# Kernel tuning notes

Measured on AMD Instinct MI355X. Metric: run time of the kernel, lower is better.

Reference implementation:

```python
import jax, jax.numpy as jnp
import numpy as np

A, B, I, H, O = 400, 64, 50, 192, 3   # num_agents, batch, input_dim, hidden_dim, output_dim
ADIM, NH = 128, 8                      # attention_dim, num_heads
HD = ADIM // NH
SCALE = HD ** -0.5
EPS = 1e-5


def _ln(x, g, b):
    mu = jnp.mean(x, -1, keepdims=True)
    v = jnp.mean((x - mu) ** 2, -1, keepdims=True)
    return (x - mu) * jax.lax.rsqrt(v + EPS) * g + b


def setup_inputs() -> dict:
    key = jax.random.key(0)
    ks = jax.random.split(key, 12)
    s = 0.05
    n = lambda k, shape: (jax.random.normal(k, shape, jnp.float32) * s)
    return {
        'x': jax.random.normal(ks[0], (B, I), jnp.float32),
        'ln_in_g': jnp.ones((A, I), jnp.float32), 'ln_in_b': jnp.zeros((A, I), jnp.float32),
        'W1': n(ks[1], (A, I, H)), 'b1': jnp.zeros((A, H), jnp.float32),
        'Ws1': n(ks[2], (A, I, H)), 'bs1': jnp.zeros((A, H), jnp.float32),
        'W2': n(ks[3], (A, H, H)), 'b2': jnp.zeros((A, H), jnp.float32),
        'Ws2': n(ks[4], (A, H, H)), 'bs2': jnp.zeros((A, H), jnp.float32),
        'W3': n(ks[5], (A, H, H)), 'b3': jnp.zeros((A, H), jnp.float32),
        'ln_h_g': jnp.ones((A, H), jnp.float32), 'ln_h_b': jnp.zeros((A, H), jnp.float32),
        'Wout': n(ks[6], (A, H, O)), 'bout': jnp.zeros((A, O), jnp.float32),
        'aln_g': jnp.ones((H,), jnp.float32), 'aln_b': jnp.zeros((H,), jnp.float32),
        'Wq': n(ks[7], (H, ADIM)), 'bq': jnp.zeros((ADIM,), jnp.float32),
        'Wk': n(ks[8], (H, ADIM)), 'bk': jnp.zeros((ADIM,), jnp.float32),
        'Wv': n(ks[9], (H, ADIM)), 'bv': jnp.zeros((ADIM,), jnp.float32),
        'Wo': n(ks[10], (ADIM, H)), 'bo': jnp.zeros((H,), jnp.float32),
    }


def _forward(x, ln_in_g, ln_in_b, W1, b1, Ws1, bs1, W2, b2, Ws2, bs2, W3, b3,
             ln_h_g, ln_h_b, Wout, bout, aln_g, aln_b, Wq, bq, Wk, bk, Wv, bv, Wo, bo):
    gelu = lambda t: jax.nn.gelu(t, approximate=False)  # torch F.gelu default = exact erf
    # per-agent input LayerNorm (shared stats, per-agent affine) -> [A, B, I]
    xn = _ln(x[None, :, :], ln_in_g[:, None, :], ln_in_b[:, None, :])
    # agent MLPs as batched GEMMs over agent axis
    h1 = gelu(jnp.einsum('abi,aih->abh', xn, W1) + b1[:, None, :]) \
         + jnp.einsum('abi,aih->abh', xn, Ws1) + bs1[:, None, :]
    h2 = gelu(jnp.einsum('abh,ahk->abk', h1, W2) + b2[:, None, :]) \
         + jnp.einsum('abh,ahk->abk', h1, Ws2) + bs2[:, None, :]
    h3 = _ln(h2 + jnp.einsum('abh,ahk->abk', h2, W3) + b3[:, None, :],
             ln_h_g[:, None, :], ln_h_b[:, None, :])  # [A, B, H]
    # cross-SREK attention across the agent axis
    y = _ln(h3, aln_g, aln_b)
    q = (y @ Wq + bq).reshape(A, B, NH, HD).transpose(1, 2, 0, 3)  # [B, NH, A, HD]
    k = (y @ Wk + bk).reshape(A, B, NH, HD).transpose(1, 2, 0, 3)
    v = (y @ Wv + bv).reshape(A, B, NH, HD).transpose(1, 2, 0, 3)
    attn = jax.nn.softmax(jnp.einsum('bhad,bhcd->bhac', q, k) * SCALE, axis=-1)
    o = jnp.einsum('bhac,bhcd->bhad', attn, v).transpose(2, 0, 1, 3).reshape(A, B, ADIM)
    attended = h3 + (o @ Wo + bo)  # residual (dropout off in eval)
    # per-agent output heads -> [A, B, O]
    logits = jnp.einsum('abh,aho->abo', attended, Wout) + bout[:, None, :]
    return logits


def reference(x, ln_in_g, ln_in_b, W1, b1, Ws1, bs1, W2, b2, Ws2, bs2, W3, b3,
              ln_h_g, ln_h_b, Wout, bout, aln_g, aln_b, Wq, bq, Wk, bk, Wv, bv, Wo, bo):
    return _forward(x, ln_in_g, ln_in_b, W1, b1, Ws1, bs1, W2, b2, Ws2, bs2, W3, b3,
                    ln_h_g, ln_h_b, Wout, bout, aln_g, aln_b, Wq, bq, Wk, bk, Wv, bv, Wo, bo)
```

## Files before the change

### kernel.cpp

```cpp
#include <hip/hip_runtime.h>
#include <math.h>

#define AGENTS 400
#define BATCH  64
#define IDIM   50
#define HDIM   192
#define ODIM   3
#define ADIMM  128
#define NHEADS 8
#define HEADD  16
#define LN_EPS 1e-5f

#define PA   200
#define PAM  192
#define POUT 136

typedef __bf16 bf16x8 __attribute__((ext_vector_type(8)));
typedef float  f32x4  __attribute__((ext_vector_type(4)));

__device__ __forceinline__ float gelu_exact(float x) {
    return 0.5f * x * (1.0f + erff(x * 0.70710678118654752f));
}

__device__ __forceinline__ unsigned pack_bf16x2(float a, float b) {
    unsigned short ua = __builtin_bit_cast(unsigned short, (__bf16)a);
    unsigned short ub = __builtin_bit_cast(unsigned short, (__bf16)b);
    return (unsigned)ua | ((unsigned)ub << 16);
}

__device__ __forceinline__ int as_swz(int row, int col) {
    return ((((col >> 3) ^ (row & 7)) << 3) | (col & 7));
}
__device__ __forceinline__ void st_as(__bf16* As_, int row, int col, float v) {
    As_[row * PAM + as_swz(row, col)] = (__bf16)v;
}
__device__ __forceinline__ float ld_as(const __bf16* As_, int row, int col) {
    return (float)As_[row * PAM + as_swz(row, col)];
}
__device__ __forceinline__ bf16x8 ld_afrag(const __bf16* As_, int row, int k0) {
    int blk = (((k0 >> 3) ^ (row & 7)) << 3);
    return *(const bf16x8*)&As_[row * PAM + blk];
}

template<int NC, int KD>
__device__ __forceinline__ void mlp_gemm2(f32x4 (&acc1)[4][3], f32x4 (&acc2)[4][3],
                                          const float* __restrict__ W,
                                          const float* __restrict__ Ws,
                                          const __bf16* As_, int n0, int lane)
{
    const int r = lane & 15, g = lane >> 4;
    const int colb[3] = { n0 + r, n0 + 16 + r, n0 + 32 + r };
    float b1f[24], b2f[24];

    #pragma unroll
    for (int t = 0; t < 3; t++)
        #pragma unroll
        for (int j = 0; j < 8; j++) {
            int k = g * 8 + j;
            int off = k * HDIM + colb[t];
            b1f[t * 8 + j] = (k < KD) ? W[off]  : 0.f;
            b2f[t * 8 + j] = (k < KD) ? Ws[off] : 0.f;
        }

    #pragma unroll
    for (int c = 0; c < NC; c++) {
        bf16x8 bf1[3], bf2[3];
        #pragma unroll
        for (int t = 0; t < 3; t++)
            #pragma unroll
            for (int j = 0; j < 8; j++) {
                bf1[t][j] = (__bf16)b1f[t * 8 + j];
                bf2[t][j] = (__bf16)b2f[t * 8 + j];
            }
        if (c + 1 < NC) {
            #pragma unroll
            for (int t = 0; t < 3; t++)
                #pragma unroll
                for (int j = 0; j < 8; j++) {
                    int k = (c + 1) * 32 + g * 8 + j;
                    int off = k * HDIM + colb[t];
                    b1f[t * 8 + j] = (k < KD) ? W[off]  : 0.f;
                    b2f[t * 8 + j] = (k < KD) ? Ws[off] : 0.f;
                }
        }
        #pragma unroll
        for (int rg = 0; rg < 4; rg++) {
            bf16x8 af = ld_afrag(As_, 16 * rg + r, c * 32 + g * 8);
            #pragma unroll
            for (int t = 0; t < 3; t++) {
                acc1[rg][t] = __builtin_amdgcn_mfma_f32_16x16x32_bf16(af, bf1[t], acc1[rg][t], 0, 0, 0);
                acc2[rg][t] = __builtin_amdgcn_mfma_f32_16x16x32_bf16(af, bf2[t], acc2[rg][t], 0, 0, 0);
            }
        }
    }
}

template<int NC, int KD>
__device__ __forceinline__ void mlp_gemm1(f32x4 (&acc)[4][3],
                                          const float* __restrict__ W,
                                          const __bf16* As_, int n0, int lane)
{
    const int r = lane & 15, g = lane >> 4;
    const int colb[3] = { n0 + r, n0 + 16 + r, n0 + 32 + r };
    float bf[24];

    #pragma unroll
    for (int t = 0; t < 3; t++)
        #pragma unroll
        for (int j = 0; j < 8; j++) {
            int k = g * 8 + j;
            bf[t * 8 + j] = (k < KD) ? W[k * HDIM + colb[t]] : 0.f;
        }

    #pragma unroll
    for (int c = 0; c < NC; c++) {
        bf16x8 bfr[3];
        #pragma unroll
        for (int t = 0; t < 3; t++)
            #pragma unroll
            for (int j = 0; j < 8; j++)
                bfr[t][j] = (__bf16)bf[t * 8 + j];
        if (c + 1 < NC) {
            #pragma unroll
            for (int t = 0; t < 3; t++)
                #pragma unroll
                for (int j = 0; j < 8; j++) {
                    int k = (c + 1) * 32 + g * 8 + j;
                    bf[t * 8 + j] = (k < KD) ? W[k * HDIM + colb[t]] : 0.f;
                }
        }
        #pragma unroll
        for (int rg = 0; rg < 4; rg++) {
            bf16x8 af = ld_afrag(As_, 16 * rg + r, c * 32 + g * 8);
            #pragma unroll
            for (int t = 0; t < 3; t++)
                acc[rg][t] = __builtin_amdgcn_mfma_f32_16x16x32_bf16(af, bfr[t], acc[rg][t], 0, 0, 0);
        }
    }
}

__global__ __launch_bounds__(256, 2) void mlp_kernel(
    const float* __restrict__ x,
    const float* __restrict__ ln_in_g, const float* __restrict__ ln_in_b,
    const float* __restrict__ W1, const float* __restrict__ b1,
    const float* __restrict__ Ws1, const float* __restrict__ bs1,
    const float* __restrict__ W2, const float* __restrict__ b2,
    const float* __restrict__ Ws2, const float* __restrict__ bs2,
    const float* __restrict__ W3, const float* __restrict__ b3,
    const float* __restrict__ ln_h_g, const float* __restrict__ ln_h_b,
    float* __restrict__ h3out)
{
    const int a    = blockIdx.x;
    const int tid  = threadIdx.x;
    const int wave = tid >> 6, lane = tid & 63;
    const int r = lane & 15, g = lane >> 4;
    const int n0 = 48 * wave;

    __shared__ __align__(16) __bf16 As[64 * PAM];
    __shared__ float mu_s[64], rs_s[64];

    {
        int rr = tid >> 2, l = tid & 3;
        float s = 0.f, ss = 0.f;
        for (int k = l; k < IDIM; k += 4) { float v = x[rr * IDIM + k]; s += v; ss += v * v; }
        s  += __shfl_down(s, 2, 4);  s  += __shfl_down(s, 1, 4);
        ss += __shfl_down(ss, 2, 4); ss += __shfl_down(ss, 1, 4);
        if (l == 0) {
            float mu = s * (1.0f / IDIM);
            float var = ss * (1.0f / IDIM) - mu * mu;
            mu_s[rr] = mu;
            rs_s[rr] = rsqrtf(var + LN_EPS);
        }
    }
    __syncthreads();
    for (int sidx = tid; sidx < 64 * 64; sidx += 256) {
        int rr = sidx >> 6, k = sidx & 63;
        float v = 0.f;
        if (k < IDIM)
            v = (x[rr * IDIM + k] - mu_s[rr]) * rs_s[rr] * ln_in_g[a * IDIM + k] + ln_in_b[a * IDIM + k];
        st_as(As, rr, k, v);
    }
    __syncthreads();

    const float* W1p  = W1  + (size_t)a * IDIM * HDIM;
    const float* Ws1p = Ws1 + (size_t)a * IDIM * HDIM;
    const float* W2p  = W2  + (size_t)a * HDIM * HDIM;
    const float* Ws2p = Ws2 + (size_t)a * HDIM * HDIM;
    const float* W3p  = W3  + (size_t)a * HDIM * HDIM;

    {
        f32x4 acc1[4][3], acc2[4][3];
        #pragma unroll
        for (int i = 0; i < 4; i++)
            #pragma unroll
            for (int t = 0; t < 3; t++) { acc1[i][t] = (f32x4)0.f; acc2[i][t] = (f32x4)0.f; }
        mlp_gemm2<2, IDIM>(acc1, acc2, W1p, Ws1p, As, n0, lane);
        __syncthreads();
        #pragma unroll
        for (int t = 0; t < 3; t++) {
            int col = n0 + 16 * t + r;
            float bb  = b1[a * HDIM + col];
            float bbs = bs1[a * HDIM + col];
            #pragma unroll
            for (int rg = 0; rg < 4; rg++)
                #pragma unroll
                for (int i = 0; i < 4; i++) {
                    int row = 16 * rg + 4 * g + i;
                    st_as(As, row, col, gelu_exact(acc1[rg][t][i] + bb) + acc2[rg][t][i] + bbs);
                }
        }
        __syncthreads();
    }

    {
        f32x4 acc1[4][3], acc2[4][3];
        #pragma unroll
        for (int i = 0; i < 4; i++)
            #pragma unroll
            for (int t = 0; t < 3; t++) { acc1[i][t] = (f32x4)0.f; acc2[i][t] = (f32x4)0.f; }
        mlp_gemm2<6, HDIM>(acc1, acc2, W2p, Ws2p, As, n0, lane);
        __syncthreads();
        #pragma unroll
        for (int t = 0; t < 3; t++) {
            int col = n0 + 16 * t + r;
            float bb  = b2[a * HDIM + col];
            float bbs = bs2[a * HDIM + col];
            #pragma unroll
            for (int rg = 0; rg < 4; rg++)
                #pragma unroll
                for (int i = 0; i < 4; i++) {
                    int row = 16 * rg + 4 * g + i;
                    st_as(As, row, col, gelu_exact(acc1[rg][t][i] + bb) + acc2[rg][t][i] + bbs);
                }
        }
        __syncthreads();
    }

    {
        f32x4 acc[4][3];
        #pragma unroll
        for (int i = 0; i < 4; i++)
            #pragma unroll
            for (int t = 0; t < 3; t++) acc[i][t] = (f32x4)0.f;
        mlp_gemm1<6, HDIM>(acc, W3p, As, n0, lane);
        __syncthreads();
        #pragma unroll
        for (int t = 0; t < 3; t++) {
            int col = n0 + 16 * t + r;
            float bb = b3[a * HDIM + col];
            #pragma unroll
            for (int rg = 0; rg < 4; rg++)
                #pragma unroll
                for (int i = 0; i < 4; i++) {
                    int row = 16 * rg + 4 * g + i;
                    st_as(As, row, col, ld_as(As, row, col) + acc[rg][t][i] + bb);
                }
        }
        __syncthreads();
    }

    {
        int rr = tid >> 2, l = tid & 3;
        float s = 0.f, ss = 0.f;
        for (int k = l; k < HDIM; k += 4) { float v = ld_as(As, rr, k); s += v; ss += v * v; }
        s  += __shfl_down(s, 2, 4);  s  += __shfl_down(s, 1, 4);
        ss += __shfl_down(ss, 2, 4); ss += __shfl_down(ss, 1, 4);
        if (l == 0) {
            float mu = s * (1.0f / HDIM);
            float var = ss * (1.0f / HDIM) - mu * mu;
            mu_s[rr] = mu;
            rs_s[rr] = rsqrtf(var + LN_EPS);
        }
    }
    __syncthreads();
    for (int sidx = tid; sidx < 64 * 48; sidx += 256) {
        int rr = sidx / 48, q = sidx - rr * 48;
        int c = q * 4;
        const __bf16* p = &As[rr * PAM + as_swz(rr, c)];
        float4 gv = *(const float4*)&ln_h_g[a * HDIM + c];
        float4 bv = *(const float4*)&ln_h_b[a * HDIM + c];
        float mu = mu_s[rr], rs = rs_s[rr];
        float4 o;
        o.x = ((float)p[0] - mu) * rs * gv.x + bv.x;
        o.y = ((float)p[1] - mu) * rs * gv.y + bv.y;
        o.z = ((float)p[2] - mu) * rs * gv.z + bv.z;
        o.w = ((float)p[3] - mu) * rs * gv.w + bv.w;
        *(float4*)&h3out[((size_t)a * BATCH + rr) * HDIM + c] = o;
    }
}

template<int NC, int KD, int NT, int NRG, int LDW, int PITCH>
__device__ __forceinline__ void gemm_bpass(f32x4 (&acc)[NRG][NT],
                                           const float* const* wptr,
                                           const __bf16* Asrc, int lane)
{
    const int r = lane & 15, g = lane >> 4;
    float buf[2][NT * 8];

    #pragma unroll
    for (int t = 0; t < NT; t++)
        #pragma unroll
        for (int j = 0; j < 8; j++) {
            int k = g * 8 + j;
            buf[0][t * 8 + j] = (k < KD) ? wptr[t][k * LDW + r] : 0.f;
        }

    #pragma unroll
    for (int c = 0; c < NC; c++) {
        const int cur = c & 1, nxt = cur ^ 1;
        if (c + 1 < NC) {
            #pragma unroll
            for (int t = 0; t < NT; t++)
                #pragma unroll
                for (int j = 0; j < 8; j++) {
                    int k = (c + 1) * 32 + g * 8 + j;
                    buf[nxt][t * 8 + j] = (k < KD) ? wptr[t][k * LDW + r] : 0.f;
                }
        }
        bf16x8 bfr[NT];
        #pragma unroll
        for (int t = 0; t < NT; t++)
            #pragma unroll
            for (int j = 0; j < 8; j++)
                bfr[t][j] = (__bf16)buf[cur][t * 8 + j];
        #pragma unroll
        for (int rg = 0; rg < NRG; rg++) {
            bf16x8 af = *(const bf16x8*)&Asrc[(16 * rg + r) * PITCH + c * 32 + g * 8];
            #pragma unroll
            for (int t = 0; t < NT; t++)
                acc[rg][t] = __builtin_amdgcn_mfma_f32_16x16x32_bf16(af, bfr[t], acc[rg][t], 0, 0, 0);
        }
    }
}

__global__ __launch_bounds__(256, 2) void qkv_kernel(
    const float* __restrict__ h3,
    const float* __restrict__ aln_g, const float* __restrict__ aln_b,
    const float* __restrict__ Wq, const float* __restrict__ bq,
    const float* __restrict__ Wk, const float* __restrict__ bk,
    const float* __restrict__ Wv, const float* __restrict__ bv,
    float* __restrict__ qT, float* __restrict__ kT, float* __restrict__ vT)
{
    const int a    = blockIdx.x;
    const int tid  = threadIdx.x;
    const int wave = tid >> 6, lane = tid & 63;
    const int r = lane & 15, g = lane >> 4;

    __shared__ __align__(16) __bf16 ys[64 * PA];
    __shared__ float mu_s[64], rs_s[64];

    {
        int rr = tid >> 2, l = tid & 3;
        const float* hp = h3 + ((size_t)a * BATCH + rr) * HDIM;
        float s = 0.f, ss = 0.f;
        for (int k = l; k < HDIM; k += 4) { float v = hp[k]; s += v; ss += v * v; }
        s  += __shfl_down(s, 2, 4);  s  += __shfl_down(s, 1, 4);
        ss += __shfl_down(ss, 2, 4); ss += __shfl_down(ss, 1, 4);
        if (l == 0) {
            float mu = s * (1.0f / HDIM);
            float var = ss * (1.0f / HDIM) - mu * mu;
            mu_s[rr] = mu;
            rs_s[rr] = rsqrtf(var + LN_EPS);
        }
    }
    __syncthreads();
    for (int sidx = tid; sidx < 64 * HDIM; sidx += 256) {
        int rr = sidx / HDIM, c = sidx - rr * HDIM;
        float v = (h3[((size_t)a * BATCH + rr) * HDIM + c] - mu_s[rr]) * rs_s[rr] * aln_g[c] + aln_b[c];
        ys[rr * PA + c] = (__bf16)v;
    }
    __syncthreads();

    #pragma unroll
    for (int p = 0; p < 2; p++) {
        const int nb = 192 * p + 48 * wave;
        const float* wA[3];
        #pragma unroll
        for (int t = 0; t < 3; t++) {
            int nt = nb + 16 * t;
            const float* base = (nt < 128) ? Wq : (nt < 256) ? Wk : Wv;
            wA[t] = base + (nt & 127);
        }
        f32x4 acc[4][3];
        #pragma unroll
        for (int i = 0; i < 4; i++)
            #pragma unroll
            for (int t = 0; t < 3; t++) acc[i][t] = (f32x4)0.f;
        gemm_bpass<6, HDIM, 3, 4, ADIMM, PA>(acc, wA, ys, lane);

        #pragma unroll
        for (int t = 0; t < 3; t++) {
            int n = nb + 16 * t + r;
            int which = n >> 7, cc = n & 127, hh = cc >> 4, dd = cc & 15;
            const float* bp = (which == 0) ? bq : (which == 1) ? bk : bv;
            float* op = (which == 0) ? qT : (which == 1) ? kT : vT;
            float bb = bp[cc];
            #pragma unroll
            for (int rg = 0; rg < 4; rg++)
                #pragma unroll
                for (int i = 0; i < 4; i++) {
                    int brow = 16 * rg + 4 * g + i;
                    op[(((size_t)brow * NHEADS + hh) * AGENTS + a) * HEADD + dd] = acc[rg][t][i] + bb;
                }
        }
    }
}

#define PKA 24
#define PVA 408
#define PPA 232

__global__ __launch_bounds__(256, 2) void attn_kernel(
    const float* __restrict__ qT, const float* __restrict__ kT,
    const float* __restrict__ vT, float* __restrict__ oT)
{
    const int bh   = blockIdx.x;
    const int b    = bh >> 3, h = bh & 7;
    const int tid  = threadIdx.x;
    const int wave = tid >> 6, lane = tid & 63;
    const int r = lane & 15, g = lane >> 4;

    __shared__ __align__(16) __bf16 Ks[AGENTS * PKA];
    __shared__ __align__(16) __bf16 Vt[16 * PVA];
    __shared__ __align__(16) __bf16 Ps[4][16 * PPA];

    const float* kp = kT + (size_t)bh * AGENTS * HEADD;
    const float* vp = vT + (size_t)bh * AGENTS * HEADD;
    for (int idx = tid; idx < AGENTS * HEADD; idx += 256) {
        int a_ = idx >> 4, d = idx & 15;
        Ks[a_ * PKA + d] = (__bf16)kp[idx];
        Vt[d * PVA + a_] = (__bf16)vp[idx];
    }
    __bf16* Pw = Ps[wave];
    for (int z = lane; z < 16 * 16; z += 64)
        Pw[(z >> 4) * PPA + 208 + (z & 15)] = (__bf16)0.f;
    __syncthreads();

    for (int mt = wave; mt < 25; mt += 4) {
        const int m0 = mt * 16;

        bf16x8 aq;
        if (g < 2) {
            const float* qp = qT + ((size_t)bh * AGENTS + m0 + r) * HEADD + g * 8;
            #pragma unroll
            for (int j = 0; j < 8; j++) aq[j] = (__bf16)(qp[j] * 0.25f);
        } else {
            #pragma unroll
            for (int j = 0; j < 8; j++) aq[j] = (__bf16)0.f;
        }

        f32x4 sacc[25];
        #pragma unroll
        for (int t = 0; t < 25; t++) {
            bf16x8 bk_ = *(const bf16x8*)&Ks[(t * 16 + r) * PKA + (g & 1) * 8];
            sacc[t] = __builtin_amdgcn_mfma_f32_16x16x32_bf16(aq, bk_, (f32x4)0.f, 0, 0, 0);
        }

        float lv[4];
        #pragma unroll
        for (int i = 0; i < 4; i++) {
            float m_ = sacc[0][i];
            #pragma unroll
            for (int t = 1; t < 25; t++) m_ = fmaxf(m_, sacc[t][i]);
            #pragma unroll
            for (int off = 8; off; off >>= 1) m_ = fmaxf(m_, __shfl_xor(m_, off, 16));
            float l_ = 0.f;
            #pragma unroll
            for (int t = 0; t < 25; t++) {
                float p = __expf(sacc[t][i] - m_);
                sacc[t][i] = p;
                l_ += p;
            }
            #pragma unroll
            for (int off = 8; off; off >>= 1) l_ += __shfl_xor(l_, off, 16);
            lv[i] = l_;
        }

        f32x4 oacc = (f32x4)0.f;

        #pragma unroll
        for (int t = 0; t < 13; t++)
            #pragma unroll
            for (int i = 0; i < 4; i++)
                Pw[(g * 4 + i) * PPA + t * 16 + r] = (__bf16)sacc[t][i];
        __asm__ volatile("s_waitcnt lgkmcnt(0)" ::: "memory");
        #pragma unroll
        for (int c = 0; c < 7; c++) {
            bf16x8 ap  = *(const bf16x8*)&Pw[r * PPA + c * 32 + g * 8];
            bf16x8 bv_ = *(const bf16x8*)&Vt[r * PVA + c * 32 + g * 8];
            oacc = __builtin_amdgcn_mfma_f32_16x16x32_bf16(ap, bv_, oacc, 0, 0, 0);
        }

        for (int z = lane; z < 16 * 16; z += 64)
            Pw[(z >> 4) * PPA + 192 + (z & 15)] = (__bf16)0.f;
        #pragma unroll
        for (int t = 13; t < 25; t++)
            #pragma unroll
            for (int i = 0; i < 4; i++)
                Pw[(g * 4 + i) * PPA + (t - 13) * 16 + r] = (__bf16)sacc[t][i];
        __asm__ volatile("s_waitcnt lgkmcnt(0)" ::: "memory");
        #pragma unroll
        for (int c = 0; c < 6; c++) {
            bf16x8 ap  = *(const bf16x8*)&Pw[r * PPA + c * 32 + g * 8];
            bf16x8 bv_ = *(const bf16x8*)&Vt[r * PVA + 208 + c * 32 + g * 8];
            oacc = __builtin_amdgcn_mfma_f32_16x16x32_bf16(ap, bv_, oacc, 0, 0, 0);
        }

        #pragma unroll
        for (int i = 0; i < 4; i++)
            oT[((size_t)(m0 + g * 4 + i) * BATCH + b) * ADIMM + h * HEADD + r] = oacc[i] / lv[i];
    }
}

__global__ __launch_bounds__(256, 2) void out_kernel(
    const float* __restrict__ h3, const float* __restrict__ oT,
    const float* __restrict__ Wo, const float* __restrict__ bo,
    const float* __restrict__ Wout, const float* __restrict__ bout,
    float* __restrict__ out)
{
    const int a    = blockIdx.x;
    const int tid  = threadIdx.x;
    const int wave = tid >> 6, lane = tid & 63;
    const int r = lane & 15, g = lane >> 4;
    const int n0 = 48 * wave;

    __shared__ __align__(16) __bf16 os[64 * POUT];
    __shared__ __align__(16) __bf16 att[64 * PA];

    for (int idx = tid; idx < 64 * 32; idx += 256) {
        int bb = idx >> 5, q = idx & 31;
        float4 v = ((const float4*)(oT + ((size_t)a * BATCH + bb) * ADIMM))[q];
        unsigned u0 = pack_bf16x2(v.x, v.y);
        unsigned u1 = pack_bf16x2(v.z, v.w);
        *(uint2*)&os[bb * POUT + q * 4] = make_uint2(u0, u1);
    }
    __syncthreads();

    {
        const float* wA[3] = { Wo + n0, Wo + n0 + 16, Wo + n0 + 32 };
        f32x4 acc[4][3];
        #pragma unroll
        for (int i = 0; i < 4; i++)
            #pragma unroll
            for (int t = 0; t < 3; t++) acc[i][t] = (f32x4)0.f;
        gemm_bpass<4, ADIMM, 3, 4, HDIM, POUT>(acc, wA, os, lane);
        #pragma unroll
        for (int t = 0; t < 3; t++) {
            int col = n0 + 16 * t + r;
            float bb = bo[col];
            #pragma unroll
            for (int rg = 0; rg < 4; rg++)
                #pragma unroll
                for (int i = 0; i < 4; i++) {
                    int row = 16 * rg + 4 * g + i;
                    float v = h3[((size_t)a * BATCH + row) * HDIM + col] + acc[rg][t][i] + bb;
                    att[row * PA + col] = (__bf16)v;
                }
        }
    }
    __syncthreads();

    {
        const float* Wp = Wout + (size_t)a * HDIM * ODIM;
        float wb[48];
        #pragma unroll
        for (int c = 0; c < 6; c++)
            #pragma unroll
            for (int j = 0; j < 8; j++) {
                int k = c * 32 + g * 8 + j;
                wb[c * 8 + j] = (r < ODIM) ? Wp[k * ODIM + r] : 0.f;
            }
        f32x4 oacc = (f32x4)0.f;
        #pragma unroll
        for (int c = 0; c < 6; c++) {
            bf16x8 bf;
            #pragma unroll
            for (int j = 0; j < 8; j++) bf[j] = (__bf16)wb[c * 8 + j];
            bf16x8 af = *(const bf16x8*)&att[(16 * wave + r) * PA + c * 32 + g * 8];
            oacc = __builtin_amdgcn_mfma_f32_16x16x32_bf16(af, bf, oacc, 0, 0, 0);
        }
        if (r < ODIM) {
            float bb = bout[a * ODIM + r];
            #pragma unroll
            for (int i = 0; i < 4; i++) {
                int row = 16 * wave + 4 * g + i;
                out[((size_t)a * BATCH + row) * ODIM + r] = oacc[i] + bb;
            }
        }
    }
}

extern "C" void kernel_launch(void* const* d_in, const int* in_sizes, int n_in,
                              void* d_out, int out_size, void* d_ws, size_t ws_size,
                              hipStream_t stream)
{
    const float* x       = (const float*)d_in[0];
    const float* ln_in_g = (const float*)d_in[1];
    const float* ln_in_b = (const float*)d_in[2];
    const float* W1      = (const float*)d_in[3];
    const float* b1      = (const float*)d_in[4];
    const float* Ws1     = (const float*)d_in[5];
    const float* bs1     = (const float*)d_in[6];
    const float* W2      = (const float*)d_in[7];
    const float* b2      = (const float*)d_in[8];
    const float* Ws2     = (const float*)d_in[9];
    const float* bs2     = (const float*)d_in[10];
    const float* W3      = (const float*)d_in[11];
    const float* b3      = (const float*)d_in[12];
    const float* ln_h_g  = (const float*)d_in[13];
    const float* ln_h_b  = (const float*)d_in[14];
    const float* Wout    = (const float*)d_in[15];
    const float* bout    = (const float*)d_in[16];
    const float* aln_g   = (const float*)d_in[17];
    const float* aln_b   = (const float*)d_in[18];
    const float* Wq      = (const float*)d_in[19];
    const float* bq      = (const float*)d_in[20];
    const float* Wk      = (const float*)d_in[21];
    const float* bk      = (const float*)d_in[22];
    const float* Wv      = (const float*)d_in[23];
    const float* bv      = (const float*)d_in[24];
    const float* Wo      = (const float*)d_in[25];
    const float* bo      = (const float*)d_in[26];
    float* out = (float*)d_out;

    float* ws = (float*)d_ws;
    const size_t H3_SZ = (size_t)AGENTS * BATCH * HDIM;
    const size_t QT_SZ = (size_t)BATCH * NHEADS * AGENTS * HEADD;
    float* h3 = ws;
    float* qT = h3 + H3_SZ;
    float* kT = qT + QT_SZ;
    float* vT = kT + QT_SZ;
    float* oT = vT + QT_SZ;

    mlp_kernel<<<AGENTS, 256, 0, stream>>>(x, ln_in_g, ln_in_b,
                                           W1, b1, Ws1, bs1, W2, b2, Ws2, bs2,
                                           W3, b3, ln_h_g, ln_h_b, h3);
    qkv_kernel<<<AGENTS, 256, 0, stream>>>(h3, aln_g, aln_b,
                                           Wq, bq, Wk, bk, Wv, bv, qT, kT, vT);
    attn_kernel<<<BATCH * NHEADS, 256, 0, stream>>>(qT, kT, vT, oT);
    out_kernel<<<AGENTS, 256, 0, stream>>>(h3, oT, Wo, bo, Wout, bout, out);
}
```

Baseline: 409.9 us.

## Stream MLP weights into double-buffered LDS via async global_load_lds

Weight tiles for all three agent MLP layers are now copied into a two-slot LDS ring with direct global-to-LDS loads, using an XOR swizzle on the column index. The load of the next 32-row tile is issued before the MFMAs on the current tile, and each step ends with a vmcnt wait and a barrier. The point is to replace per-lane strided register prefetch of weights with wide, coalesced async copies and to lower register pressure. In exchange the block uses about 48KB more shared memory and synchronises after every slot, which may limit occupancy and overlap.

```diff
diff --git a/kernel.cpp b/kernel.cpp
--- a/kernel.cpp
+++ b/kernel.cpp
@@ -42,100 +42,53 @@
     return *(const bf16x8*)&As_[row * PAM + blk];
 }
 
-template<int NC, int KD>
-__device__ __forceinline__ void mlp_gemm2(f32x4 (&acc1)[4][3], f32x4 (&acc2)[4][3],
-                                          const float* __restrict__ W,
-                                          const float* __restrict__ Ws,
-                                          const __bf16* As_, int n0, int lane)
+#define VMWAIT0()   do { asm volatile("s_waitcnt vmcnt(0)" ::: "memory"); \
+                         __builtin_amdgcn_sched_barrier(0); } while (0)
+#define BARRIER()   do { __builtin_amdgcn_s_barrier(); \
+                         __builtin_amdgcn_sched_barrier(0); } while (0)
+
+struct WPtrs { const float *W1, *Ws1, *W2, *Ws2, *W3; };
+
+__device__ __forceinline__ void issue_slot(int s, float* buf0, float* buf1,
+                                           const WPtrs& P, const int* kloc,
+                                           const int* nsw, int tid)
+{
+    const float* M; int c, kdm1;
+    if (s < 4)       { M = (s & 1) ? P.Ws1 : P.W1; c = s >> 1;      kdm1 = IDIM - 1; }
+    else if (s < 16) { int u = s - 4; M = (u & 1) ? P.Ws2 : P.W2; c = u >> 1; kdm1 = HDIM - 1; }
+    else             { M = P.W3; c = s - 16; kdm1 = HDIM - 1; }
+    float* dst = (s & 1) ? buf1 : buf0;
+    #pragma unroll
+    for (int i = 0; i < 6; i++) {
+        int kg = c * 32 + kloc[i];
+        kg = (kg <= kdm1) ? kg : kdm1;
+        const float* src = M + (size_t)kg * HDIM + nsw[i];
+        __builtin_amdgcn_global_load_lds(
+            (const __attribute__((address_space(1))) void*)src,
+            (__attribute__((address_space(3))) void*)(dst + (i * 256 + tid) * 4),
+            16, 0, 0);
+    }
+    __builtin_amdgcn_sched_barrier(0);
+}
+
+__device__ __forceinline__ void slot_mfma_f32(f32x4 (&acc)[4][3], const __bf16* As_,
+                                              const float* Wbuf, int c, int n0, int lane)
 {
     const int r = lane & 15, g = lane >> 4;
-    const int colb[3] = { n0 + r, n0 + 16 + r, n0 + 32 + r };
-    float b1f[24], b2f[24];
-
+    bf16x8 bf[3];
     #pragma unroll
-    for (int t = 0; t < 3; t++)
-        #pragma unroll
-        for (int j = 0; j < 8; j++) {
-            int k = g * 8 + j;
-            int off = k * HDIM + colb[t];
-            b1f[t * 8 + j] = (k < KD) ? W[off]  : 0.f;
-            b2f[t * 8 + j] = (k < KD) ? Ws[off] : 0.f;
-        }
-
+    for (int t = 0; t < 3; t++) {
+        int cs = (n0 + 16 * t + r) ^ (g << 3);
+        #pragma unroll
+        for (int j = 0; j < 8; j++)
+            bf[t][j] = (__bf16)Wbuf[(g * 8 + j) * HDIM + cs];
+    }
     #pragma unroll
-    for (int c = 0; c < NC; c++) {
-        bf16x8 bf1[3], bf2[3];
+    for (int rg = 0; rg < 4; rg++) {
+        bf16x8 af = ld_afrag(As_, 16 * rg + r, c * 32 + g * 8);
         #pragma unroll
         for (int t = 0; t < 3; t++)
-            #pragma unroll
-            for (int j = 0; j < 8; j++) {
-                bf1[t][j] = (__bf16)b1f[t * 8 + j];
-                bf2[t][j] = (__bf16)b2f[t * 8 + j];
-            }
-        if (c + 1 < NC) {
-            #pragma unroll
-            for (int t = 0; t < 3; t++)
-                #pragma unroll
-                for (int j = 0; j < 8; j++) {
-                    int k = (c + 1) * 32 + g * 8 + j;
-                    int off = k * HDIM + colb[t];
-                    b1f[t * 8 + j] = (k < KD) ? W[off]  : 0.f;
-                    b2f[t * 8 + j] = (k < KD) ? Ws[off] : 0.f;
-                }
-        }
-        #pragma unroll
-        for (int rg = 0; rg < 4; rg++) {
-            bf16x8 af = ld_afrag(As_, 16 * rg + r, c * 32 + g * 8);
-            #pragma unroll
-            for (int t = 0; t < 3; t++) {
-                acc1[rg][t] = __builtin_amdgcn_mfma_f32_16x16x32_bf16(af, bf1[t], acc1[rg][t], 0, 0, 0);
-                acc2[rg][t] = __builtin_amdgcn_mfma_f32_16x16x32_bf16(af, bf2[t], acc2[rg][t], 0, 0, 0);
-            }
-        }
-    }
-}
-
-template<int NC, int KD>
-__device__ __forceinline__ void mlp_gemm1(f32x4 (&acc)[4][3],
-                                          const float* __restrict__ W,
-                                          const __bf16* As_, int n0, int lane)
-{
-    const int r = lane & 15, g = lane >> 4;
-    const int colb[3] = { n0 + r, n0 + 16 + r, n0 + 32 + r };
-    float bf[24];
-
-    #pragma unroll
-    for (int t = 0; t < 3; t++)
-        #pragma unroll
-        for (int j = 0; j < 8; j++) {
-            int k = g * 8 + j;
-            bf[t * 8 + j] = (k < KD) ? W[k * HDIM + colb[t]] : 0.f;
-        }
-
-    #pragma unroll
-    for (int c = 0; c < NC; c++) {
-        bf16x8 bfr[3];
-        #pragma unroll
-        for (int t = 0; t < 3; t++)
-            #pragma unroll
-            for (int j = 0; j < 8; j++)
-                bfr[t][j] = (__bf16)bf[t * 8 + j];
-        if (c + 1 < NC) {
-            #pragma unroll
-            for (int t = 0; t < 3; t++)
-                #pragma unroll
-                for (int j = 0; j < 8; j++) {
-                    int k = (c + 1) * 32 + g * 8 + j;
-                    bf[t * 8 + j] = (k < KD) ? W[k * HDIM + colb[t]] : 0.f;
-                }
-        }
-        #pragma unroll
-        for (int rg = 0; rg < 4; rg++) {
-            bf16x8 af = ld_afrag(As_, 16 * rg + r, c * 32 + g * 8);
-            #pragma unroll
-            for (int t = 0; t < 3; t++)
-                acc[rg][t] = __builtin_amdgcn_mfma_f32_16x16x32_bf16(af, bfr[t], acc[rg][t], 0, 0, 0);
-        }
+            acc[rg][t] = __builtin_amdgcn_mfma_f32_16x16x32_bf16(af, bf[t], acc[rg][t], 0, 0, 0);
     }
 }
 
@@ -157,7 +110,24 @@
     const int n0 = 48 * wave;
 
     __shared__ __align__(16) __bf16 As[64 * PAM];
+    __shared__ __align__(16) float  Wbuf[2][32 * HDIM];
     __shared__ float mu_s[64], rs_s[64];
+
+    int kloc[6], nsw[6];
+    #pragma unroll
+    for (int i = 0; i < 6; i++) {
+        int w = i * 1024 + tid * 4;
+        kloc[i] = w / HDIM;
+        int np = w - kloc[i] * HDIM;
+        nsw[i] = np ^ (((kloc[i] >> 3) & 3) << 3);
+    }
+
+    const WPtrs P = {
+        W1  + (size_t)a * IDIM * HDIM,
+        Ws1 + (size_t)a * IDIM * HDIM,
+        W2  + (size_t)a * HDIM * HDIM,
+        Ws2 + (size_t)a * HDIM * HDIM,
+        W3  + (size_t)a * HDIM * HDIM };
 
     {
         int rr = tid >> 2, l = tid & 3;
@@ -173,6 +143,9 @@
         }
     }
     __syncthreads();
+
+    issue_slot(0, Wbuf[0], Wbuf[1], P, kloc, nsw, tid);
+
     for (int sidx = tid; sidx < 64 * 64; sidx += 256) {
         int rr = sidx >> 6, k = sidx & 63;
         float v = 0.f;
@@ -182,20 +155,21 @@
     }
     __syncthreads();
 
-    const float* W1p  = W1  + (size_t)a * IDIM * HDIM;
-    const float* Ws1p = Ws1 + (size_t)a * IDIM * HDIM;
-    const float* W2p  = W2  + (size_t)a * HDIM * HDIM;
-    const float* Ws2p = Ws2 + (size_t)a * HDIM * HDIM;
-    const float* W3p  = W3  + (size_t)a * HDIM * HDIM;
-
     {
         f32x4 acc1[4][3], acc2[4][3];
         #pragma unroll
         for (int i = 0; i < 4; i++)
             #pragma unroll
             for (int t = 0; t < 3; t++) { acc1[i][t] = (f32x4)0.f; acc2[i][t] = (f32x4)0.f; }
-        mlp_gemm2<2, IDIM>(acc1, acc2, W1p, Ws1p, As, n0, lane);
-        __syncthreads();
+        #pragma unroll
+        for (int s = 0; s < 4; s++) {
+            if (s < 3) issue_slot(s + 1, Wbuf[0], Wbuf[1], P, kloc, nsw, tid);
+            if ((s & 1) == 0) slot_mfma_f32(acc1, As, Wbuf[s & 1], s >> 1, n0, lane);
+            else              slot_mfma_f32(acc2, As, Wbuf[s & 1], s >> 1, n0, lane);
+            VMWAIT0();
+            BARRIER();
+        }
+        issue_slot(4, Wbuf[0], Wbuf[1], P, kloc, nsw, tid);
         #pragma unroll
         for (int t = 0; t < 3; t++) {
             int col = n0 + 16 * t + r;
@@ -218,8 +192,15 @@
         for (int i = 0; i < 4; i++)
             #pragma unroll
             for (int t = 0; t < 3; t++) { acc1[i][t] = (f32x4)0.f; acc2[i][t] = (f32x4)0.f; }
-        mlp_gemm2<6, HDIM>(acc1, acc2, W2p, Ws2p, As, n0, lane);
-        __syncthreads();
+        #pragma unroll
+        for (int s = 4; s < 16; s++) {
+            if (s < 15) issue_slot(s + 1, Wbuf[0], Wbuf[1], P, kloc, nsw, tid);
+            if ((s & 1) == 0) slot_mfma_f32(acc1, As, Wbuf[s & 1], (s - 4) >> 1, n0, lane);
+            else              slot_mfma_f32(acc2, As, Wbuf[s & 1], (s - 4) >> 1, n0, lane);
+            VMWAIT0();
+            BARRIER();
+        }
+        issue_slot(16, Wbuf[0], Wbuf[1], P, kloc, nsw, tid);
         #pragma unroll
         for (int t = 0; t < 3; t++) {
             int col = n0 + 16 * t + r;
@@ -242,8 +223,13 @@
         for (int i = 0; i < 4; i++)
             #pragma unroll
             for (int t = 0; t < 3; t++) acc[i][t] = (f32x4)0.f;
-        mlp_gemm1<6, HDIM>(acc, W3p, As, n0, lane);
-        __syncthreads();
+        #pragma unroll
+        for (int s = 16; s < 22; s++) {
+            if (s < 21) issue_slot(s + 1, Wbuf[0], Wbuf[1], P, kloc, nsw, tid);
+            slot_mfma_f32(acc, As, Wbuf[s & 1], s - 16, n0, lane);
+            VMWAIT0();
+            BARRIER();
+        }
         #pragma unroll
         for (int t = 0; t < 3; t++) {
             int col = n0 + 16 * t + r;
```

Measured after the change: 360.4 us. -12.1%, faster.
